# Optimization experiments

Hardware: AMD Instinct MI355X
Metric: run time of the kernel (lower is better)

The kernel has to match this reference:

```python
import jax, jax.numpy as jnp
import numpy as np

MIN_NORM = 1e-15
N = 10000        # num_nodes
E = 320000       # num edges (avg degree 32)
F_IN = 512       # in_features
HID = 256        # hardcoded encoder hidden dim
D_HYP = 2        # Poincare embedding dim
HEIGHT = 2
MAX_SIZE = 0.999
MIN_SCALE = HEIGHT * (MAX_SIZE / (HEIGHT + 1))  # = 0.666, scale clamp lower bound
MAX_SCALE = MAX_SIZE


def setup_inputs() -> dict:
    key = jax.random.key(0)
    ks = jax.random.split(key, 5)
    feature = jax.random.normal(ks[0], (N, F_IN), jnp.float32)
    edge_index = jax.random.randint(ks[1], (2, E), 0, N, dtype=jnp.int64)
    W1 = jax.random.normal(ks[2], (F_IN, HID), jnp.float32) / np.sqrt(F_IN).astype(np.float32)
    b1 = jnp.zeros((HID,), jnp.float32)
    W2 = jax.random.normal(ks[3], (HID, D_HYP), jnp.float32) / np.sqrt(HID).astype(np.float32)
    b2 = jnp.zeros((D_HYP,), jnp.float32)
    scale = jnp.ones((1,), jnp.float32)  # init_size overridden to 1.0 in __init__
    return {"feature": feature, "edge_index": edge_index, "W1": W1, "b1": b1,
            "W2": W2, "b2": b2, "scale": scale}


def _gcn_agg(h, src, dst):
    # symmetric-normalized edge_index gather/aggregate (message passing)
    deg = jax.ops.segment_sum(jnp.ones((src.shape[0],), h.dtype), dst, num_segments=N)
    deg = jnp.maximum(deg, 1.0)
    norm = jax.lax.rsqrt(deg[src] * deg[dst])            # [E]
    msg = h[src] * norm[:, None]                          # [E, C] gather (irregular)
    return jax.ops.segment_sum(msg, dst, num_segments=N)  # [N, C] scatter-add


def reference(feature, edge_index, W1, b1, W2, b2, scale):
    src, dst = edge_index[0], edge_index[1]
    # 2-layer graph encoder (linear -> aggregate -> relu, linear -> aggregate)
    h = jax.nn.relu(_gcn_agg(feature @ W1 + b1, src, dst))   # [N, HID]
    u = _gcn_agg(h @ W2 + b2, src, dst)                      # [N, D_HYP] tangent at origin
    # lift to Lorentz model (k=-1) via expmap0: x = [cosh|u|, sinh|u| * u/|u|]
    un = jnp.maximum(jnp.linalg.norm(u, axis=-1, keepdims=True), MIN_NORM)
    x_l = jnp.concatenate([jnp.cosh(un), jnp.sinh(un) * u / un], axis=-1)  # [N, D_HYP+1]
    # Lorentz -> Poincare: p = x_space / (1 + x_time)
    p = x_l[:, 1:] / (1.0 + x_l[:, :1])
    # normalize: F.normalize(p, dim=-1) * scale.clamp(min_size, max_size)
    pn = jnp.maximum(jnp.linalg.norm(p, axis=-1, keepdims=True), 1e-12)
    s = jnp.clip(scale, MIN_SCALE, MAX_SCALE)
    p = p / pn * s
    # project onto Poincare ball of curvature k=-1 with eps=MIN_NORM
    norm = jnp.maximum(jnp.linalg.norm(p, axis=-1, keepdims=True), MIN_NORM)
    maxnorm = 1.0 - MIN_NORM
    return jnp.where(norm > maxnorm, p / norm * maxnorm, p)
```

## Files before the change

kernel.cpp:

```cpp
#include <hip/hip_runtime.h>
#include <math.h>

#define N_NODES 10000
#define N_EDGES 320000
#define F_IN 512
#define HID 256
#define PAD_DEG 80
#define LDSTR 40

typedef _Float16 half8 __attribute__((ext_vector_type(8)));
typedef float floatx4 __attribute__((ext_vector_type(4)));

__device__ __forceinline__ void fma4(float4& acc, float s, const float4& v) {
    acc.x += s * v.x; acc.y += s * v.y; acc.z += s * v.z; acc.w += s * v.w;
}


__global__ void k_build(const int* __restrict__ ei, int* __restrict__ count,
                        int* __restrict__ csr) {
    int e = blockIdx.x * blockDim.x + threadIdx.x;
    if (e >= N_EDGES) return;
    int src = ei[e];
    int dst = ei[N_EDGES + e];
    int pos = atomicAdd(&count[dst], 1);
    csr[dst * PAD_DEG + pos] = src;
}


__global__ void k_prep(const float* __restrict__ W1, _Float16* __restrict__ Bt_hi,
                       _Float16* __restrict__ Bt_lo, const int* __restrict__ csr,
                       const int* __restrict__ count, float* __restrict__ wcsr) {
    int idx = blockIdx.x * blockDim.x + threadIdx.x;
    if (idx < F_IN * HID) {
        int k = idx >> 8, n = idx & 255;
        float v = W1[idx];
        _Float16 hi = (_Float16)v;
        _Float16 lo = (_Float16)(v - (float)hi);
        Bt_hi[n * F_IN + k] = hi;
        Bt_lo[n * F_IN + k] = lo;
    }
    if (idx < N_NODES * PAD_DEG) {
        int n = idx / PAD_DEG, j = idx - n * PAD_DEG;
        int deg = count[n];
        if (j < deg) {
            int s = csr[idx];
            int cs = count[s];
            wcsr[idx] = rsqrtf((float)((cs > 0 ? cs : 1) * deg));
        }
    }
}


__global__ __launch_bounds__(256) void k_gemm(const float* __restrict__ A,
                                              const _Float16* __restrict__ Bt_hi,
                                              const _Float16* __restrict__ Bt_lo,
                                              const float* __restrict__ b1,
                                              float* __restrict__ h0) {
    __shared__ _Float16 As_hi[64 * LDSTR], As_lo[64 * LDSTR];
    __shared__ _Float16 Bs_hi[64 * LDSTR], Bs_lo[64 * LDSTR];
    int tid = threadIdx.x;
    int row0 = blockIdx.y * 64, col0 = blockIdx.x * 64;
    int r = tid >> 2, c = (tid & 3) << 3;
    int lane = tid & 63, w = tid >> 6;
    int wm = (w >> 1) * 32, wn = (w & 1) * 32;
    int quad = lane >> 4, l15 = lane & 15;
    floatx4 acc[2][2] = {};

    for (int k0 = 0; k0 < F_IN; k0 += 32) {
        float av[8];
        int arow = row0 + r;
        if (arow < N_NODES) {
            float4 v0 = *(const float4*)(A + (size_t)arow * F_IN + k0 + c);
            float4 v1 = *(const float4*)(A + (size_t)arow * F_IN + k0 + c + 4);
            av[0] = v0.x; av[1] = v0.y; av[2] = v0.z; av[3] = v0.w;
            av[4] = v1.x; av[5] = v1.y; av[6] = v1.z; av[7] = v1.w;
        } else {
            #pragma unroll
            for (int i = 0; i < 8; ++i) av[i] = 0.f;
        }
        half8 hhi, hlo;
        #pragma unroll
        for (int i = 0; i < 8; ++i) {
            _Float16 h = (_Float16)av[i];
            hhi[i] = h;
            hlo[i] = (_Float16)(av[i] - (float)h);
        }
        *(half8*)&As_hi[r * LDSTR + c] = hhi;
        *(half8*)&As_lo[r * LDSTR + c] = hlo;
        *(half8*)&Bs_hi[r * LDSTR + c] = *(const half8*)(Bt_hi + (size_t)(col0 + r) * F_IN + k0 + c);
        *(half8*)&Bs_lo[r * LDSTR + c] = *(const half8*)(Bt_lo + (size_t)(col0 + r) * F_IN + k0 + c);
        __syncthreads();

        half8 a_hi[2], a_lo[2], b_hi[2], b_lo[2];
        #pragma unroll
        for (int mi = 0; mi < 2; ++mi) {
            int mr = wm + mi * 16 + l15;
            a_hi[mi] = *(half8*)&As_hi[mr * LDSTR + quad * 8];
            a_lo[mi] = *(half8*)&As_lo[mr * LDSTR + quad * 8];
        }
        #pragma unroll
        for (int ni = 0; ni < 2; ++ni) {
            int nr = wn + ni * 16 + l15;
            b_hi[ni] = *(half8*)&Bs_hi[nr * LDSTR + quad * 8];
            b_lo[ni] = *(half8*)&Bs_lo[nr * LDSTR + quad * 8];
        }
        #pragma unroll
        for (int mi = 0; mi < 2; ++mi)
            #pragma unroll
            for (int ni = 0; ni < 2; ++ni) {
                acc[mi][ni] = __builtin_amdgcn_mfma_f32_16x16x32_f16(a_hi[mi], b_hi[ni], acc[mi][ni], 0, 0, 0);
                acc[mi][ni] = __builtin_amdgcn_mfma_f32_16x16x32_f16(a_hi[mi], b_lo[ni], acc[mi][ni], 0, 0, 0);
                acc[mi][ni] = __builtin_amdgcn_mfma_f32_16x16x32_f16(a_lo[mi], b_hi[ni], acc[mi][ni], 0, 0, 0);
            }
        __syncthreads();
    }
    #pragma unroll
    for (int mi = 0; mi < 2; ++mi)
        #pragma unroll
        for (int ni = 0; ni < 2; ++ni) {
            int colb = col0 + wn + ni * 16 + l15;
            float bias = b1[colb];
            #pragma unroll
            for (int reg = 0; reg < 4; ++reg) {
                int rowb = row0 + wm + mi * 16 + quad * 4 + reg;
                if (rowb < N_NODES) h0[(size_t)rowb * HID + colb] = acc[mi][ni][reg] + bias;
            }
        }
}


__global__ __launch_bounds__(256) void k_agg1(const float* __restrict__ h0,
                                              const int* __restrict__ csr,
                                              const float* __restrict__ wcsr,
                                              const int* __restrict__ count,
                                              const float* __restrict__ W2,
                                              const float* __restrict__ b2,
                                              float* __restrict__ u0) {
    int n = blockIdx.x * 4 + (threadIdx.x >> 6);
    int lane = threadIdx.x & 63;
    if (n >= N_NODES) return;
    int deg = count[n];
    const int*   row  = csr  + (size_t)n * PAD_DEG;
    const float* wrow = wcsr + (size_t)n * PAD_DEG;
    int off = lane << 2;
    float4 acc0 = {0,0,0,0}, acc1 = {0,0,0,0}, acc2 = {0,0,0,0}, acc3 = {0,0,0,0};
    int j = 0;
    for (; j + 8 <= deg; j += 8) {
        int s0 = row[j+0], s1 = row[j+1], s2 = row[j+2], s3 = row[j+3];
        int s4 = row[j+4], s5 = row[j+5], s6 = row[j+6], s7 = row[j+7];
        float w0 = wrow[j+0], w1 = wrow[j+1], w2 = wrow[j+2], w3 = wrow[j+3];
        float w4 = wrow[j+4], w5 = wrow[j+5], w6 = wrow[j+6], w7 = wrow[j+7];
        float4 v0 = *(const float4*)(h0 + (size_t)s0 * HID + off);
        float4 v1 = *(const float4*)(h0 + (size_t)s1 * HID + off);
        float4 v2 = *(const float4*)(h0 + (size_t)s2 * HID + off);
        float4 v3 = *(const float4*)(h0 + (size_t)s3 * HID + off);
        float4 v4 = *(const float4*)(h0 + (size_t)s4 * HID + off);
        float4 v5 = *(const float4*)(h0 + (size_t)s5 * HID + off);
        float4 v6 = *(const float4*)(h0 + (size_t)s6 * HID + off);
        float4 v7 = *(const float4*)(h0 + (size_t)s7 * HID + off);
        fma4(acc0, w0, v0); fma4(acc1, w1, v1); fma4(acc2, w2, v2); fma4(acc3, w3, v3);
        fma4(acc0, w4, v4); fma4(acc1, w5, v5); fma4(acc2, w6, v6); fma4(acc3, w7, v7);
    }
    for (; j < deg; ++j) {
        int s = row[j];
        float wq = wrow[j];
        float4 v = *(const float4*)(h0 + (size_t)s * HID + off);
        fma4(acc0, wq, v);
    }
    acc0.x += acc1.x + acc2.x + acc3.x;
    acc0.y += acc1.y + acc2.y + acc3.y;
    acc0.z += acc1.z + acc2.z + acc3.z;
    acc0.w += acc1.w + acc2.w + acc3.w;
    acc0.x = fmaxf(acc0.x, 0.f); acc0.y = fmaxf(acc0.y, 0.f);
    acc0.z = fmaxf(acc0.z, 0.f); acc0.w = fmaxf(acc0.w, 0.f);
    float4 wa = *(const float4*)(W2 + (lane << 3));
    float4 wb = *(const float4*)(W2 + (lane << 3) + 4);
    float p0 = acc0.x * wa.x + acc0.y * wa.z + acc0.z * wb.x + acc0.w * wb.z;
    float p1 = acc0.x * wa.y + acc0.y * wa.w + acc0.z * wb.y + acc0.w * wb.w;
    #pragma unroll
    for (int o = 32; o > 0; o >>= 1) {
        p0 += __shfl_down(p0, o);
        p1 += __shfl_down(p1, o);
    }
    if (lane == 0) {
        u0[2 * n]     = p0 + b2[0];
        u0[2 * n + 1] = p1 + b2[1];
    }
}


__global__ __launch_bounds__(256) void k_agg2(const float* __restrict__ u0,
                                              const int* __restrict__ csr,
                                              const float* __restrict__ wcsr,
                                              const int* __restrict__ count,
                                              const float* __restrict__ scale,
                                              float* __restrict__ out) {
    int n = blockIdx.x * 4 + (threadIdx.x >> 6);
    int lane = threadIdx.x & 63;
    if (n >= N_NODES) return;
    int deg = count[n];
    const int*   row  = csr  + (size_t)n * PAD_DEG;
    const float* wrow = wcsr + (size_t)n * PAD_DEG;
    float a0 = 0.f, a1 = 0.f;
    for (int j = lane; j < deg; j += 64) {
        int s = row[j];
        float wq = wrow[j];
        float2 uv = *(const float2*)(u0 + 2 * (size_t)s);
        a0 += wq * uv.x;
        a1 += wq * uv.y;
    }
    #pragma unroll
    for (int o = 32; o > 0; o >>= 1) {
        a0 += __shfl_down(a0, o);
        a1 += __shfl_down(a1, o);
    }
    if (lane == 0) {
        float un = fmaxf(sqrtf(a0 * a0 + a1 * a1), 1e-15f);
        float t = tanhf(0.5f * un) / un;
        float p0 = a0 * t, p1 = a1 * t;
        float pn = fmaxf(sqrtf(p0 * p0 + p1 * p1), 1e-12f);
        float s = fminf(fmaxf(scale[0], 0.666f), 0.999f);
        p0 = p0 / pn * s; p1 = p1 / pn * s;
        float nn = fmaxf(sqrtf(p0 * p0 + p1 * p1), 1e-15f);
        if (nn > 1.0f) { p0 = p0 / nn; p1 = p1 / nn; }
        out[2 * n]     = p0;
        out[2 * n + 1] = p1;
    }
}


extern "C" void kernel_launch(void* const* d_in, const int* in_sizes, int n_in,
                              void* d_out, int out_size, void* d_ws, size_t ws_size,
                              hipStream_t stream) {
    const float* feature = (const float*)d_in[0];
    const int*   ei      = (const int*)d_in[1];
    const float* W1      = (const float*)d_in[2];
    const float* b1      = (const float*)d_in[3];
    const float* W2      = (const float*)d_in[4];
    const float* b2      = (const float*)d_in[5];
    const float* scale   = (const float*)d_in[6];
    float* out = (float*)d_out;

    char* W = (char*)d_ws;
    int*      count = (int*)W;
    int*      csr   = (int*)(W + 40960);
    float*    wcsr  = (float*)(W + 3240960);
    float*    h0    = (float*)(W + 6440960);
    float*    u0    = (float*)(W + 16680960);
    _Float16* Bt_hi = (_Float16*)(W + 16760960);
    _Float16* Bt_lo = (_Float16*)(W + 17023104);

    (void)hipMemsetAsync(count, 0, 10240 * sizeof(int), stream);

    k_build<<<dim3((N_EDGES + 255) / 256), dim3(256), 0, stream>>>(ei, count, csr);
    k_prep<<<dim3((N_NODES * PAD_DEG + 255) / 256), dim3(256), 0, stream>>>(W1, Bt_hi, Bt_lo, csr, count, wcsr);
    k_gemm<<<dim3(HID / 64, (N_NODES + 63) / 64), dim3(256), 0, stream>>>(feature, Bt_hi, Bt_lo, b1, h0);
    k_agg1<<<dim3((N_NODES + 3) / 4), dim3(256), 0, stream>>>(h0, csr, wcsr, count, W2, b2, u0);
    k_agg2<<<dim3((N_NODES + 3) / 4), dim3(256), 0, stream>>>(u0, csr, wcsr, count, scale, out);
}
```

Baseline: 163.4 us.

## Precompute fp16 hi/lo split of features in build kernel before GEMM

Moves the fp32-to-fp16 hi/lo split of the feature matrix out of the GEMM inner loop into the graph-build kernel, which also absorbs the W1 conversion. The GEMM then loads pre-split fp16 tiles directly and uses a 1D tile order so the four column tiles sharing a row block are adjacent. This removes repeated conversion work per column tile but adds a full extra write and read of the split feature matrix through memory.

```diff
diff --git a/kernel.cpp b/kernel.cpp
--- a/kernel.cpp
+++ b/kernel.cpp
@@ -7,6 +7,9 @@
 #define HID 256
 #define PAD_DEG 80
 #define LDSTR 40
+#define N_TILES (157 * 4)
+#define A_ROWS 10048
+#define A_CHUNKS (A_ROWS * F_IN / 8)
 
 typedef _Float16 half8 __attribute__((ext_vector_type(8)));
 typedef float floatx4 __attribute__((ext_vector_type(4)));
@@ -16,81 +19,86 @@
 }
 
 
-__global__ void k_build(const int* __restrict__ ei, int* __restrict__ count,
-                        int* __restrict__ csr) {
-    int e = blockIdx.x * blockDim.x + threadIdx.x;
-    if (e >= N_EDGES) return;
-    int src = ei[e];
-    int dst = ei[N_EDGES + e];
-    int pos = atomicAdd(&count[dst], 1);
-    csr[dst * PAD_DEG + pos] = src;
-}
-
-
-__global__ void k_prep(const float* __restrict__ W1, _Float16* __restrict__ Bt_hi,
-                       _Float16* __restrict__ Bt_lo, const int* __restrict__ csr,
-                       const int* __restrict__ count, float* __restrict__ wcsr) {
+__global__ void k_build(const int* __restrict__ ei, const float* __restrict__ feature,
+                        const float* __restrict__ W1, int* __restrict__ count,
+                        int* __restrict__ csr, _Float16* __restrict__ A_hi,
+                        _Float16* __restrict__ A_lo, _Float16* __restrict__ Bt_hi,
+                        _Float16* __restrict__ Bt_lo) {
+    int i = blockIdx.x * blockDim.x + threadIdx.x;
+    if (i < A_CHUNKS) {
+        int row = i >> 6;
+        half8 hhi, hlo;
+        if (row < N_NODES) {
+            const float* src = feature + (size_t)i * 8;
+            float4 v0 = *(const float4*)src;
+            float4 v1 = *(const float4*)(src + 4);
+            float av[8] = {v0.x, v0.y, v0.z, v0.w, v1.x, v1.y, v1.z, v1.w};
+            #pragma unroll
+            for (int t = 0; t < 8; ++t) {
+                _Float16 h = (_Float16)av[t];
+                hhi[t] = h;
+                hlo[t] = (_Float16)(av[t] - (float)h);
+            }
+        } else {
+            #pragma unroll
+            for (int t = 0; t < 8; ++t) { hhi[t] = (_Float16)0.f; hlo[t] = (_Float16)0.f; }
+        }
+        *(half8*)(A_hi + (size_t)i * 8) = hhi;
+        *(half8*)(A_lo + (size_t)i * 8) = hlo;
+    }
+    if (i < F_IN * HID) {
+        int k = i >> 8, n = i & 255;
+        float v = W1[i];
+        _Float16 hi = (_Float16)v;
+        Bt_hi[n * F_IN + k] = hi;
+        Bt_lo[n * F_IN + k] = (_Float16)(v - (float)hi);
+    }
+    if (i < N_EDGES) {
+        int src = ei[i];
+        int dst = ei[N_EDGES + i];
+        int pos = atomicAdd(&count[dst], 1);
+        csr[dst * PAD_DEG + pos] = src;
+    }
+}
+
+
+__global__ void k_prep(const int* __restrict__ csr, const int* __restrict__ count,
+                       float* __restrict__ wcsr) {
     int idx = blockIdx.x * blockDim.x + threadIdx.x;
-    if (idx < F_IN * HID) {
-        int k = idx >> 8, n = idx & 255;
-        float v = W1[idx];
-        _Float16 hi = (_Float16)v;
-        _Float16 lo = (_Float16)(v - (float)hi);
-        Bt_hi[n * F_IN + k] = hi;
-        Bt_lo[n * F_IN + k] = lo;
-    }
-    if (idx < N_NODES * PAD_DEG) {
-        int n = idx / PAD_DEG, j = idx - n * PAD_DEG;
-        int deg = count[n];
-        if (j < deg) {
-            int s = csr[idx];
-            int cs = count[s];
-            wcsr[idx] = rsqrtf((float)((cs > 0 ? cs : 1) * deg));
-        }
-    }
-}
-
-
-__global__ __launch_bounds__(256) void k_gemm(const float* __restrict__ A,
+    if (idx >= N_NODES * PAD_DEG) return;
+    int n = idx / PAD_DEG, j = idx - n * PAD_DEG;
+    int deg = count[n];
+    if (j < deg) {
+        int s = csr[idx];
+        int cs = count[s];
+        wcsr[idx] = rsqrtf((float)((cs > 0 ? cs : 1) * deg));
+    }
+}
+
+
+__global__ __launch_bounds__(256) void k_gemm(const _Float16* __restrict__ A_hi,
+                                              const _Float16* __restrict__ A_lo,
                                               const _Float16* __restrict__ Bt_hi,
                                               const _Float16* __restrict__ Bt_lo,
                                               const float* __restrict__ b1,
                                               float* __restrict__ h0) {
     __shared__ _Float16 As_hi[64 * LDSTR], As_lo[64 * LDSTR];
     __shared__ _Float16 Bs_hi[64 * LDSTR], Bs_lo[64 * LDSTR];
-    int tid = threadIdx.x;
-    int row0 = blockIdx.y * 64, col0 = blockIdx.x * 64;
-    int r = tid >> 2, c = (tid & 3) << 3;
-    int lane = tid & 63, w = tid >> 6;
-    int wm = (w >> 1) * 32, wn = (w & 1) * 32;
-    int quad = lane >> 4, l15 = lane & 15;
+    const int tid = threadIdx.x;
+    const int lane = tid & 63, w = tid >> 6;
+    const int wm = (w >> 1) * 32, wn = (w & 1) * 32;
+    const int quad = lane >> 4, l15 = lane & 15;
+    const int r = tid >> 2, c = (tid & 3) << 3;
+    const int t = blockIdx.x;
+    const int row0 = (t >> 2) * 64, col0 = (t & 3) * 64;
     floatx4 acc[2][2] = {};
 
     for (int k0 = 0; k0 < F_IN; k0 += 32) {
-        float av[8];
-        int arow = row0 + r;
-        if (arow < N_NODES) {
-            float4 v0 = *(const float4*)(A + (size_t)arow * F_IN + k0 + c);
-            float4 v1 = *(const float4*)(A + (size_t)arow * F_IN + k0 + c + 4);
-            av[0] = v0.x; av[1] = v0.y; av[2] = v0.z; av[3] = v0.w;
-            av[4] = v1.x; av[5] = v1.y; av[6] = v1.z; av[7] = v1.w;
-        } else {
-            #pragma unroll
-            for (int i = 0; i < 8; ++i) av[i] = 0.f;
-        }
-        half8 hhi, hlo;
-        #pragma unroll
-        for (int i = 0; i < 8; ++i) {
-            _Float16 h = (_Float16)av[i];
-            hhi[i] = h;
-            hlo[i] = (_Float16)(av[i] - (float)h);
-        }
-        *(half8*)&As_hi[r * LDSTR + c] = hhi;
-        *(half8*)&As_lo[r * LDSTR + c] = hlo;
+        *(half8*)&As_hi[r * LDSTR + c] = *(const half8*)(A_hi + (size_t)(row0 + r) * F_IN + k0 + c);
+        *(half8*)&As_lo[r * LDSTR + c] = *(const half8*)(A_lo + (size_t)(row0 + r) * F_IN + k0 + c);
         *(half8*)&Bs_hi[r * LDSTR + c] = *(const half8*)(Bt_hi + (size_t)(col0 + r) * F_IN + k0 + c);
         *(half8*)&Bs_lo[r * LDSTR + c] = *(const half8*)(Bt_lo + (size_t)(col0 + r) * F_IN + k0 + c);
         __syncthreads();
-
         half8 a_hi[2], a_lo[2], b_hi[2], b_lo[2];
         #pragma unroll
         for (int mi = 0; mi < 2; ++mi) {
@@ -162,10 +170,8 @@
         fma4(acc0, w4, v4); fma4(acc1, w5, v5); fma4(acc2, w6, v6); fma4(acc3, w7, v7);
     }
     for (; j < deg; ++j) {
-        int s = row[j];
-        float wq = wrow[j];
-        float4 v = *(const float4*)(h0 + (size_t)s * HID + off);
-        fma4(acc0, wq, v);
+        float4 v = *(const float4*)(h0 + (size_t)row[j] * HID + off);
+        fma4(acc0, wrow[j], v);
     }
     acc0.x += acc1.x + acc2.x + acc3.x;
     acc0.y += acc1.y + acc2.y + acc3.y;
@@ -203,9 +209,8 @@
     const float* wrow = wcsr + (size_t)n * PAD_DEG;
     float a0 = 0.f, a1 = 0.f;
     for (int j = lane; j < deg; j += 64) {
-        int s = row[j];
         float wq = wrow[j];
-        float2 uv = *(const float2*)(u0 + 2 * (size_t)s);
+        float2 uv = *(const float2*)(u0 + 2 * (size_t)row[j]);
         a0 += wq * uv.x;
         a1 += wq * uv.y;
     }
@@ -249,12 +254,15 @@
     float*    u0    = (float*)(W + 16680960);
     _Float16* Bt_hi = (_Float16*)(W + 16760960);
     _Float16* Bt_lo = (_Float16*)(W + 17023104);
+    _Float16* A_hi  = (_Float16*)(W + 17285248);
+    _Float16* A_lo  = (_Float16*)(W + 27574400);
 
     (void)hipMemsetAsync(count, 0, 10240 * sizeof(int), stream);
 
-    k_build<<<dim3((N_EDGES + 255) / 256), dim3(256), 0, stream>>>(ei, count, csr);
-    k_prep<<<dim3((N_NODES * PAD_DEG + 255) / 256), dim3(256), 0, stream>>>(W1, Bt_hi, Bt_lo, csr, count, wcsr);
-    k_gemm<<<dim3(HID / 64, (N_NODES + 63) / 64), dim3(256), 0, stream>>>(feature, Bt_hi, Bt_lo, b1, h0);
+    k_build<<<dim3((A_CHUNKS + 255) / 256), dim3(256), 0, stream>>>(
+        ei, feature, W1, count, csr, A_hi, A_lo, Bt_hi, Bt_lo);
+    k_prep<<<dim3((N_NODES * PAD_DEG + 255) / 256), dim3(256), 0, stream>>>(csr, count, wcsr);
+    k_gemm<<<dim3(N_TILES), dim3(256), 0, stream>>>(A_hi, A_lo, Bt_hi, Bt_lo, b1, h0);
     k_agg1<<<dim3((N_NODES + 3) / 4), dim3(256), 0, stream>>>(h0, csr, wcsr, count, W2, b2, u0);
     k_agg2<<<dim3((N_NODES + 3) / 4), dim3(256), 0, stream>>>(u0, csr, wcsr, count, scale, out);
 }
```

Measured after the change: 168.6 us. 1.03x slower.

## Drop precomputed edge-weight array; compute norms inline and merge prep into build

Applied to the files above, without the earlier changes.

Removes the k_prep kernel and the wcsr edge-weight buffer. Each aggregation now computes rsqrt(deg_src*deg_dst) on the fly from the count array, and the W1 fp16 hi/lo split moves into the k_build kernel. The gemm grid is flattened to 1D with column tiles innermost. This saves one launch and a full write-then-read pass over the padded weight array, at the cost of extra gathered count loads and rsqrt work in the aggregation loops.

```diff
diff --git a/kernel.cpp b/kernel.cpp
--- a/kernel.cpp
+++ b/kernel.cpp
@@ -7,6 +7,7 @@
 #define HID 256
 #define PAD_DEG 80
 #define LDSTR 40
+#define N_TILES (157 * 4)
 
 typedef _Float16 half8 __attribute__((ext_vector_type(8)));
 typedef float floatx4 __attribute__((ext_vector_type(4)));
@@ -16,37 +17,22 @@
 }
 
 
-__global__ void k_build(const int* __restrict__ ei, int* __restrict__ count,
-                        int* __restrict__ csr) {
-    int e = blockIdx.x * blockDim.x + threadIdx.x;
-    if (e >= N_EDGES) return;
-    int src = ei[e];
-    int dst = ei[N_EDGES + e];
-    int pos = atomicAdd(&count[dst], 1);
-    csr[dst * PAD_DEG + pos] = src;
-}
-
-
-__global__ void k_prep(const float* __restrict__ W1, _Float16* __restrict__ Bt_hi,
-                       _Float16* __restrict__ Bt_lo, const int* __restrict__ csr,
-                       const int* __restrict__ count, float* __restrict__ wcsr) {
-    int idx = blockIdx.x * blockDim.x + threadIdx.x;
-    if (idx < F_IN * HID) {
-        int k = idx >> 8, n = idx & 255;
-        float v = W1[idx];
+__global__ void k_build(const int* __restrict__ ei, const float* __restrict__ W1,
+                        int* __restrict__ count, int* __restrict__ csr,
+                        _Float16* __restrict__ Bt_hi, _Float16* __restrict__ Bt_lo) {
+    int i = blockIdx.x * blockDim.x + threadIdx.x;
+    if (i < F_IN * HID) {
+        int k = i >> 8, n = i & 255;
+        float v = W1[i];
         _Float16 hi = (_Float16)v;
-        _Float16 lo = (_Float16)(v - (float)hi);
         Bt_hi[n * F_IN + k] = hi;
-        Bt_lo[n * F_IN + k] = lo;
-    }
-    if (idx < N_NODES * PAD_DEG) {
-        int n = idx / PAD_DEG, j = idx - n * PAD_DEG;
-        int deg = count[n];
-        if (j < deg) {
-            int s = csr[idx];
-            int cs = count[s];
-            wcsr[idx] = rsqrtf((float)((cs > 0 ? cs : 1) * deg));
-        }
+        Bt_lo[n * F_IN + k] = (_Float16)(v - (float)hi);
+    }
+    if (i < N_EDGES) {
+        int src = ei[i];
+        int dst = ei[N_EDGES + i];
+        int pos = atomicAdd(&count[dst], 1);
+        csr[dst * PAD_DEG + pos] = src;
     }
 }
 
@@ -58,12 +44,13 @@
                                               float* __restrict__ h0) {
     __shared__ _Float16 As_hi[64 * LDSTR], As_lo[64 * LDSTR];
     __shared__ _Float16 Bs_hi[64 * LDSTR], Bs_lo[64 * LDSTR];
-    int tid = threadIdx.x;
-    int row0 = blockIdx.y * 64, col0 = blockIdx.x * 64;
-    int r = tid >> 2, c = (tid & 3) << 3;
-    int lane = tid & 63, w = tid >> 6;
-    int wm = (w >> 1) * 32, wn = (w & 1) * 32;
-    int quad = lane >> 4, l15 = lane & 15;
+    const int tid = threadIdx.x;
+    const int lane = tid & 63, w = tid >> 6;
+    const int wm = (w >> 1) * 32, wn = (w & 1) * 32;
+    const int quad = lane >> 4, l15 = lane & 15;
+    const int r = tid >> 2, c = (tid & 3) << 3;
+    const int t = blockIdx.x;
+    const int row0 = (t >> 2) * 64, col0 = (t & 3) * 64;
     floatx4 acc[2][2] = {};
 
     for (int k0 = 0; k0 < F_IN; k0 += 32) {
@@ -90,7 +77,6 @@
         *(half8*)&Bs_hi[r * LDSTR + c] = *(const half8*)(Bt_hi + (size_t)(col0 + r) * F_IN + k0 + c);
         *(half8*)&Bs_lo[r * LDSTR + c] = *(const half8*)(Bt_lo + (size_t)(col0 + r) * F_IN + k0 + c);
         __syncthreads();
-
         half8 a_hi[2], a_lo[2], b_hi[2], b_lo[2];
         #pragma unroll
         for (int mi = 0; mi < 2; ++mi) {
@@ -131,7 +117,6 @@
 
 __global__ __launch_bounds__(256) void k_agg1(const float* __restrict__ h0,
                                               const int* __restrict__ csr,
-                                              const float* __restrict__ wcsr,
                                               const int* __restrict__ count,
                                               const float* __restrict__ W2,
                                               const float* __restrict__ b2,
@@ -140,16 +125,16 @@
     int lane = threadIdx.x & 63;
     if (n >= N_NODES) return;
     int deg = count[n];
-    const int*   row  = csr  + (size_t)n * PAD_DEG;
-    const float* wrow = wcsr + (size_t)n * PAD_DEG;
+    float degd = (float)(deg > 0 ? deg : 1);
+    const int* row = csr + (size_t)n * PAD_DEG;
     int off = lane << 2;
     float4 acc0 = {0,0,0,0}, acc1 = {0,0,0,0}, acc2 = {0,0,0,0}, acc3 = {0,0,0,0};
     int j = 0;
     for (; j + 8 <= deg; j += 8) {
         int s0 = row[j+0], s1 = row[j+1], s2 = row[j+2], s3 = row[j+3];
         int s4 = row[j+4], s5 = row[j+5], s6 = row[j+6], s7 = row[j+7];
-        float w0 = wrow[j+0], w1 = wrow[j+1], w2 = wrow[j+2], w3 = wrow[j+3];
-        float w4 = wrow[j+4], w5 = wrow[j+5], w6 = wrow[j+6], w7 = wrow[j+7];
+        int c0 = count[s0], c1 = count[s1], c2 = count[s2], c3 = count[s3];
+        int c4 = count[s4], c5 = count[s5], c6 = count[s6], c7 = count[s7];
         float4 v0 = *(const float4*)(h0 + (size_t)s0 * HID + off);
         float4 v1 = *(const float4*)(h0 + (size_t)s1 * HID + off);
         float4 v2 = *(const float4*)(h0 + (size_t)s2 * HID + off);
@@ -158,14 +143,20 @@
         float4 v5 = *(const float4*)(h0 + (size_t)s5 * HID + off);
         float4 v6 = *(const float4*)(h0 + (size_t)s6 * HID + off);
         float4 v7 = *(const float4*)(h0 + (size_t)s7 * HID + off);
-        fma4(acc0, w0, v0); fma4(acc1, w1, v1); fma4(acc2, w2, v2); fma4(acc3, w3, v3);
-        fma4(acc0, w4, v4); fma4(acc1, w5, v5); fma4(acc2, w6, v6); fma4(acc3, w7, v7);
+        fma4(acc0, rsqrtf((float)(c0 > 0 ? c0 : 1) * degd), v0);
+        fma4(acc1, rsqrtf((float)(c1 > 0 ? c1 : 1) * degd), v1);
+        fma4(acc2, rsqrtf((float)(c2 > 0 ? c2 : 1) * degd), v2);
+        fma4(acc3, rsqrtf((float)(c3 > 0 ? c3 : 1) * degd), v3);
+        fma4(acc0, rsqrtf((float)(c4 > 0 ? c4 : 1) * degd), v4);
+        fma4(acc1, rsqrtf((float)(c5 > 0 ? c5 : 1) * degd), v5);
+        fma4(acc2, rsqrtf((float)(c6 > 0 ? c6 : 1) * degd), v6);
+        fma4(acc3, rsqrtf((float)(c7 > 0 ? c7 : 1) * degd), v7);
     }
     for (; j < deg; ++j) {
         int s = row[j];
-        float wq = wrow[j];
+        int cs = count[s];
         float4 v = *(const float4*)(h0 + (size_t)s * HID + off);
-        fma4(acc0, wq, v);
+        fma4(acc0, rsqrtf((float)(cs > 0 ? cs : 1) * degd), v);
     }
     acc0.x += acc1.x + acc2.x + acc3.x;
     acc0.y += acc1.y + acc2.y + acc3.y;
@@ -191,7 +182,6 @@
 
 __global__ __launch_bounds__(256) void k_agg2(const float* __restrict__ u0,
                                               const int* __restrict__ csr,
-                                              const float* __restrict__ wcsr,
                                               const int* __restrict__ count,
                                               const float* __restrict__ scale,
                                               float* __restrict__ out) {
@@ -199,12 +189,13 @@
     int lane = threadIdx.x & 63;
     if (n >= N_NODES) return;
     int deg = count[n];
-    const int*   row  = csr  + (size_t)n * PAD_DEG;
-    const float* wrow = wcsr + (size_t)n * PAD_DEG;
+    float degd = (float)(deg > 0 ? deg : 1);
+    const int* row = csr + (size_t)n * PAD_DEG;
     float a0 = 0.f, a1 = 0.f;
     for (int j = lane; j < deg; j += 64) {
         int s = row[j];
-        float wq = wrow[j];
+        int cs = count[s];
+        float wq = rsqrtf((float)(cs > 0 ? cs : 1) * degd);
         float2 uv = *(const float2*)(u0 + 2 * (size_t)s);
         a0 += wq * uv.x;
         a1 += wq * uv.y;
@@ -244,17 +235,16 @@
     char* W = (char*)d_ws;
     int*      count = (int*)W;
     int*      csr   = (int*)(W + 40960);
-    float*    wcsr  = (float*)(W + 3240960);
-    float*    h0    = (float*)(W + 6440960);
-    float*    u0    = (float*)(W + 16680960);
-    _Float16* Bt_hi = (_Float16*)(W + 16760960);
-    _Float16* Bt_lo = (_Float16*)(W + 17023104);
+    float*    h0    = (float*)(W + 3240960);
+    float*    u0    = (float*)(W + 13480960);
+    _Float16* Bt_hi = (_Float16*)(W + 13560960);
+    _Float16* Bt_lo = (_Float16*)(W + 13823104);
 
     (void)hipMemsetAsync(count, 0, 10240 * sizeof(int), stream);
 
-    k_build<<<dim3((N_EDGES + 255) / 256), dim3(256), 0, stream>>>(ei, count, csr);
-    k_prep<<<dim3((N_NODES * PAD_DEG + 255) / 256), dim3(256), 0, stream>>>(W1, Bt_hi, Bt_lo, csr, count, wcsr);
-    k_gemm<<<dim3(HID / 64, (N_NODES + 63) / 64), dim3(256), 0, stream>>>(feature, Bt_hi, Bt_lo, b1, h0);
-    k_agg1<<<dim3((N_NODES + 3) / 4), dim3(256), 0, stream>>>(h0, csr, wcsr, count, W2, b2, u0);
-    k_agg2<<<dim3((N_NODES + 3) / 4), dim3(256), 0, stream>>>(u0, csr, wcsr, count, scale, out);
-}
+    k_build<<<dim3((N_EDGES + 255) / 256), dim3(256), 0, stream>>>(
+        ei, W1, count, csr, Bt_hi, Bt_lo);
+    k_gemm<<<dim3(N_TILES), dim3(256), 0, stream>>>(feature, Bt_hi, Bt_lo, b1, h0);
+    k_agg1<<<dim3((N_NODES + 3) / 4), dim3(256), 0, stream>>>(h0, csr, count, W2, b2, u0);
+    k_agg2<<<dim3((N_NODES + 3) / 4), dim3(256), 0, stream>>>(u0, csr, count, scale, out);
+}
```

Result: faster. 158.9 us (-2.7%).
